# Kernel tuning notes

Hardware: AMD Instinct MI355X
Metric: run time of the kernel (lower is better)

The kernel has to match this reference:

```python
import jax, jax.numpy as jnp
import numpy as np

B, P, E = 256, 196, 2048           # batch, num_pixels, encoder_size
H, A, EMB = 2048, 512, 300         # hidden, attention, embedding dims
V_IN, V_OUT = 262, 261             # input vocab (classes+2), output (classes+1)
T = 7                              # max_seq_len + 2


def setup_inputs() -> dict:
    key = jax.random.key(0)
    ks = jax.random.split(key, 20)
    s = 0.02
    return {
        "encoder_feature_out": jax.random.normal(ks[0], (B, P, E), jnp.float32),
        "encoder_out": jax.random.normal(ks[1], (B, E), jnp.float32),
        "annotations_X": jax.random.randint(ks[2], (B, T), 0, V_IN),
        "is_train": 1,
        "emb_W": jax.random.normal(ks[3], (V_IN, EMB), jnp.float32) * s,
        "feat_W": jax.random.normal(ks[4], (H, E), jnp.float32) * s,
        "feat_b": jnp.zeros((H,), jnp.float32),
        "W_ih": jax.random.normal(ks[5], (4 * H, EMB + E), jnp.float32) * s,
        "W_hh": jax.random.normal(ks[6], (4 * H, H), jnp.float32) * s,
        "b_ih": jnp.zeros((4 * H,), jnp.float32),
        "b_hh": jnp.zeros((4 * H,), jnp.float32),
        "enc_att_W": jax.random.normal(ks[7], (A, E), jnp.float32) * s,
        "enc_att_b": jnp.zeros((A,), jnp.float32),
        "dec_att_W": jax.random.normal(ks[8], (A, H), jnp.float32) * s,
        "dec_att_b": jnp.zeros((A,), jnp.float32),
        "full_att_W": jax.random.normal(ks[9], (1, A), jnp.float32) * s,
        "full_att_b": jnp.zeros((1,), jnp.float32),
        "fbeta_W": jax.random.normal(ks[10], (E, H), jnp.float32) * s,
        "fbeta_b": jnp.zeros((E,), jnp.float32),
        "fc_W": jax.random.normal(ks[11], (V_OUT, H), jnp.float32) * s,
        "fc_b": jnp.zeros((V_OUT,), jnp.float32),
    }


def _forward(encoder_feature_out, encoder_out, annotations_X,
             emb_W, feat_W, feat_b, W_ih, W_hh, b_ih, b_hh,
             enc_att_W, enc_att_b, dec_att_W, dec_att_b,
             full_att_W, full_att_b, fbeta_W, fbeta_b, fc_W, fc_b):
    enc = encoder_feature_out                                  # (B,P,E)
    # encoder side of additive attention is constant across steps
    att1 = jnp.einsum('bpe,ae->bpa', enc, enc_att_W) + enc_att_b  # (B,P,A)
    h0 = encoder_out @ feat_W.T + feat_b                       # (B,H)
    c0 = jnp.zeros_like(h0)

    def step(carry, ann_t):
        h, c = carry
        # additive attention
        att2 = h @ dec_att_W.T + dec_att_b                     # (B,A)
        e = jax.nn.relu(att1 + att2[:, None, :]) @ full_att_W[0] + full_att_b[0]  # (B,P)
        alpha = jax.nn.softmax(e, axis=1)                      # (B,P)
        awe = jnp.einsum('bp,bpe->be', alpha, enc)             # (B,E)
        gate = jax.nn.sigmoid(h @ fbeta_W.T + fbeta_b)         # (B,E)
        awe = gate * awe
        # LSTMCell (dropout layers in eval mode -> identity)
        x = jnp.concatenate([emb_W[ann_t], awe], axis=1)       # (B,EMB+E)
        gates = x @ W_ih.T + b_ih + h @ W_hh.T + b_hh          # (B,4H)
        i, f, g, o = jnp.split(gates, 4, axis=1)
        c = jax.nn.sigmoid(f) * c + jax.nn.sigmoid(i) * jnp.tanh(g)
        h = jax.nn.sigmoid(o) * jnp.tanh(c)
        yhat = h @ fc_W.T + fc_b                               # (B,V_OUT)
        return (h, c), (yhat, alpha)

    _, (yhats, alphas) = jax.lax.scan(step, (h0, c0), annotations_X.T)  # (T,B,...)
    return jnp.transpose(yhats, (1, 0, 2)), jnp.transpose(alphas, (1, 0, 2))


def reference(encoder_feature_out, encoder_out, annotations_X, is_train,
              emb_W, feat_W, feat_b, W_ih, W_hh, b_ih, b_hh,
              enc_att_W, enc_att_b, dec_att_W, dec_att_b,
              full_att_W, full_att_b, fbeta_W, fbeta_b, fc_W, fc_b):
    # is_train=True (teacher forcing) path
    return _forward(encoder_feature_out, encoder_out, annotations_X,
                    emb_W, feat_W, feat_b, W_ih, W_hh, b_ih, b_hh,
                    enc_att_W, enc_att_b, dec_att_W, dec_att_b,
                    full_att_W, full_att_b, fbeta_W, fbeta_b, fc_W, fc_b)
```

## Files before the change

kernel.cpp:

```cpp
#include <hip/hip_runtime.h>
#include <math.h>

#define B_    256
#define P_    196
#define E_    2048
#define H_    2048
#define A_    512
#define EMB_  300
#define VOUT_ 261
#define T_    7

#define KPAD_   4480
#define EMBOFF_ 2048
#define AWEOFF_ 2348
#define KREAL_  4396

#define NSTEP_  2880
#define FCN_    320

typedef __attribute__((ext_vector_type(8))) short          short8_t;
typedef __attribute__((ext_vector_type(8))) unsigned short ushort8_t;
typedef __attribute__((ext_vector_type(4))) float          f32x4;

__device__ __forceinline__ unsigned short f2b(float f) {
    union { float f; unsigned int u; } v; v.f = f;
    unsigned int x = v.u;
    unsigned int r = (x + 0x7fffu + ((x >> 16) & 1u)) >> 16;
    return (unsigned short)r;
}
__device__ __forceinline__ float b2f(unsigned short u) {
    union { unsigned int u; float f; } v; v.u = ((unsigned int)u) << 16;
    return v.f;
}

__global__ __launch_bounds__(256)
void gemm_skinny(const unsigned short* __restrict__ Ab, int lda,
                 const unsigned short* __restrict__ Bw, int ldb,
                 float* __restrict__ Cpart, int N, int Kper)
{
    __shared__ ushort8_t As8[256 * 8];
    __shared__ ushort8_t Bs8[64 * 8];

    const int tid  = threadIdx.x;
    const int lane = tid & 63;
    const int w    = tid >> 6;
    const int col0 = blockIdx.x * 64;
    const int kbase = blockIdx.y * Kper;
    float* __restrict__ Cs = Cpart + (size_t)blockIdx.y * 256 * N;

    const int rb  = tid >> 3;
    const int seg = tid & 7;
    const int swz = seg ^ (rb & 7);

    const unsigned short* Ap = Ab + (size_t)rb * lda + kbase + seg * 8;
    const unsigned short* Bp = Bw + (size_t)(col0 + rb) * ldb + kbase + seg * 8;

    const int lr = lane & 15;
    const int hi = lane >> 4;

    f32x4 acc[4][4];
    #pragma unroll
    for (int m = 0; m < 4; ++m)
        #pragma unroll
        for (int n = 0; n < 4; ++n)
            acc[m][n] = (f32x4){0.f, 0.f, 0.f, 0.f};

    ushort8_t aR[8], bR[2];
    #pragma unroll
    for (int i = 0; i < 8; ++i)
        aR[i] = *(const ushort8_t*)(Ap + (size_t)i * 32 * lda);
    bR[0] = *(const ushort8_t*)(Bp);
    bR[1] = *(const ushort8_t*)(Bp + (size_t)32 * ldb);

    for (int k0 = 0; k0 < Kper; k0 += 64) {
        __syncthreads();
        #pragma unroll
        for (int i = 0; i < 8; ++i)
            As8[(rb + i * 32) * 8 + swz] = aR[i];
        Bs8[rb * 8 + swz]        = bR[0];
        Bs8[(rb + 32) * 8 + swz] = bR[1];
        __syncthreads();
        if (k0 + 64 < Kper) {
            #pragma unroll
            for (int i = 0; i < 8; ++i)
                aR[i] = *(const ushort8_t*)(Ap + (size_t)i * 32 * lda + k0 + 64);
            bR[0] = *(const ushort8_t*)(Bp + k0 + 64);
            bR[1] = *(const ushort8_t*)(Bp + (size_t)32 * ldb + k0 + 64);
        }
        #pragma unroll
        for (int kc = 0; kc < 2; ++kc) {
            short8_t af[4], bf[4];
            #pragma unroll
            for (int m = 0; m < 4; ++m) {
                const int row = w * 64 + m * 16 + lr;
                af[m] = *(const short8_t*)&As8[row * 8 + ((kc * 4 + hi) ^ (row & 7))];
            }
            #pragma unroll
            for (int n = 0; n < 4; ++n) {
                const int row = n * 16 + lr;
                bf[n] = *(const short8_t*)&Bs8[row * 8 + ((kc * 4 + hi) ^ (row & 7))];
            }
            #pragma unroll
            for (int m = 0; m < 4; ++m)
                #pragma unroll
                for (int n = 0; n < 4; ++n)
                    acc[m][n] = __builtin_amdgcn_mfma_f32_16x16x32_bf16(
                        af[m], bf[n], acc[m][n], 0, 0, 0);
        }
    }

    #pragma unroll
    for (int m = 0; m < 4; ++m) {
        const int grow0 = w * 64 + m * 16 + hi * 4;
        #pragma unroll
        for (int n = 0; n < 4; ++n) {
            const int gcol = col0 + n * 16 + lr;
            #pragma unroll
            for (int r = 0; r < 4; ++r)
                Cs[(size_t)(grow0 + r) * N + gcol] = acc[m][n][r];
        }
    }
}

template<bool ABF16>
__global__ __launch_bounds__(256)
void gemm_mfma(const void* __restrict__ Ap, int lda,
               const unsigned short* __restrict__ Bw, int ldb,
               unsigned short* __restrict__ Cp, int ldc,
               const float* __restrict__ bias,
               int M, int N, int K)
{
    __shared__ __align__(16) unsigned short As[64][40];
    __shared__ __align__(16) unsigned short Bs[128][40];

    const int tid  = threadIdx.x;
    const int lane = tid & 63;
    const int wid  = tid >> 6;
    const int wr   = wid >> 1;
    const int wc   = wid & 1;
    const int row0 = blockIdx.y * 64;
    const int col0 = blockIdx.x * 128;

    const int ar = tid >> 2;
    const int as = (tid & 3) * 8;
    const int br = tid >> 1;
    const int bs = (tid & 1) * 16;

    const int lr = lane & 15;
    const int lk = (lane >> 4) * 8;

    f32x4 acc[2][4];
    #pragma unroll
    for (int m = 0; m < 2; ++m)
        #pragma unroll
        for (int n = 0; n < 4; ++n)
            acc[m][n] = (f32x4){0.f, 0.f, 0.f, 0.f};

    for (int k0 = 0; k0 < K; k0 += 32) {
        ushort8_t aval = {0,0,0,0,0,0,0,0};
        if (row0 + ar < M) {
            if (ABF16) {
                const unsigned short* A16 = (const unsigned short*)Ap;
                aval = *(const ushort8_t*)(A16 + (size_t)(row0 + ar) * lda + k0 + as);
            } else {
                const float* Af = (const float*)Ap;
                const float* p = Af + (size_t)(row0 + ar) * lda + k0 + as;
                float4 v0 = *(const float4*)(p);
                float4 v1 = *(const float4*)(p + 4);
                aval[0] = f2b(v0.x); aval[1] = f2b(v0.y);
                aval[2] = f2b(v0.z); aval[3] = f2b(v0.w);
                aval[4] = f2b(v1.x); aval[5] = f2b(v1.y);
                aval[6] = f2b(v1.z); aval[7] = f2b(v1.w);
            }
        }
        ushort8_t bv0 = {0,0,0,0,0,0,0,0}, bv1 = {0,0,0,0,0,0,0,0};
        if (col0 + br < N) {
            const unsigned short* p = Bw + (size_t)(col0 + br) * ldb + k0 + bs;
            bv0 = *(const ushort8_t*)(p);
            bv1 = *(const ushort8_t*)(p + 8);
        }
        __syncthreads();
        *(ushort8_t*)&As[ar][as]     = aval;
        *(ushort8_t*)&Bs[br][bs]     = bv0;
        *(ushort8_t*)&Bs[br][bs + 8] = bv1;
        __syncthreads();

        short8_t af[2], bf[4];
        #pragma unroll
        for (int m = 0; m < 2; ++m)
            af[m] = *(const short8_t*)&As[wr * 32 + m * 16 + lr][lk];
        #pragma unroll
        for (int n = 0; n < 4; ++n)
            bf[n] = *(const short8_t*)&Bs[wc * 64 + n * 16 + lr][lk];
        #pragma unroll
        for (int m = 0; m < 2; ++m)
            #pragma unroll
            for (int n = 0; n < 4; ++n)
                acc[m][n] = __builtin_amdgcn_mfma_f32_16x16x32_bf16(
                    af[m], bf[n], acc[m][n], 0, 0, 0);
    }

    #pragma unroll
    for (int m = 0; m < 2; ++m) {
        const int grow0 = row0 + wr * 32 + m * 16 + (lane >> 4) * 4;
        #pragma unroll
        for (int n = 0; n < 4; ++n) {
            const int gcol = col0 + wc * 64 + n * 16 + lr;
            if (gcol >= N) continue;
            const float bv = bias[gcol];
            #pragma unroll
            for (int r = 0; r < 4; ++r) {
                const int grow = grow0 + r;
                if (grow >= M) continue;
                Cp[(size_t)grow * ldc + gcol] = f2b(acc[m][n][r] + bv);
            }
        }
    }
}

__global__ __launch_bounds__(256)
void cvt_bf16_kernel(const float* __restrict__ in, unsigned short* __restrict__ out,
                     int n8)
{
    const int idx = blockIdx.x * 256 + threadIdx.x;
    if (idx >= n8) return;
    const size_t base = (size_t)idx * 8;
    float4 v0 = *(const float4*)(in + base);
    float4 v1 = *(const float4*)(in + base + 4);
    ushort8_t u;
    u[0]=f2b(v0.x); u[1]=f2b(v0.y); u[2]=f2b(v0.z); u[3]=f2b(v0.w);
    u[4]=f2b(v1.x); u[5]=f2b(v1.y); u[6]=f2b(v1.z); u[7]=f2b(v1.w);
    *(ushort8_t*)(out + base) = u;
}

__global__ __launch_bounds__(256)
void build_wcat_kernel(const float* __restrict__ W_ih, const float* __restrict__ W_hh,
                       unsigned short* __restrict__ wcat)
{
    const int row = blockIdx.x;
    for (int s = threadIdx.x; s < KPAD_ / 8; s += 256) {
        const int k0 = s * 8;
        ushort8_t u;
        if (k0 + 8 <= H_) {
            const float* p = W_hh + (size_t)row * H_ + k0;
            float4 v0 = *(const float4*)(p);
            float4 v1 = *(const float4*)(p + 4);
            u[0]=f2b(v0.x); u[1]=f2b(v0.y); u[2]=f2b(v0.z); u[3]=f2b(v0.w);
            u[4]=f2b(v1.x); u[5]=f2b(v1.y); u[6]=f2b(v1.z); u[7]=f2b(v1.w);
        } else if (k0 >= H_ && k0 + 8 <= KREAL_) {
            const float* p = W_ih + (size_t)row * (EMB_ + E_) + (k0 - H_);
            float4 v0 = *(const float4*)(p);
            float4 v1 = *(const float4*)(p + 4);
            u[0]=f2b(v0.x); u[1]=f2b(v0.y); u[2]=f2b(v0.z); u[3]=f2b(v0.w);
            u[4]=f2b(v1.x); u[5]=f2b(v1.y); u[6]=f2b(v1.z); u[7]=f2b(v1.w);
        } else {
            #pragma unroll
            for (int i = 0; i < 8; ++i) {
                const int k = k0 + i;
                float v = 0.f;
                if (k < KREAL_ && k >= H_) v = W_ih[(size_t)row * (EMB_ + E_) + (k - H_)];
                u[i] = f2b(v);
            }
        }
        *(ushort8_t*)(wcat + (size_t)row * KPAD_ + k0) = u;
    }
}

__global__ __launch_bounds__(256)
void build_wstep_kernel(const float* __restrict__ dec_attW,
                        const float* __restrict__ fbeta_W,
                        const float* __restrict__ fc_W,
                        unsigned short* __restrict__ wstep)
{
    const int row = blockIdx.x;
    const int c0  = threadIdx.x * 8;
    const float* src;
    if (row < A_)                 src = dec_attW + (size_t)row * H_ + c0;
    else if (row < A_ + E_)       src = fbeta_W + (size_t)(row - A_) * H_ + c0;
    else if (row < A_ + E_ + VOUT_) src = fc_W + (size_t)(row - A_ - E_) * H_ + c0;
    else                          src = nullptr;
    ushort8_t u = {0,0,0,0,0,0,0,0};
    if (src) {
        float4 v0 = *(const float4*)(src);
        float4 v1 = *(const float4*)(src + 4);
        u[0]=f2b(v0.x); u[1]=f2b(v0.y); u[2]=f2b(v0.z); u[3]=f2b(v0.w);
        u[4]=f2b(v1.x); u[5]=f2b(v1.y); u[6]=f2b(v1.z); u[7]=f2b(v1.w);
    }
    *(ushort8_t*)(wstep + (size_t)row * H_ + c0) = u;
}

__global__ __launch_bounds__(256)
void reduce_step(const float* __restrict__ parts, float* __restrict__ att2,
                 float* __restrict__ gatelin, float* __restrict__ outy,
                 const float* __restrict__ dec_attb, const float* __restrict__ fbeta_b,
                 const float* __restrict__ fc_b, int t)
{
    const int i = blockIdx.x * 256 + threadIdx.x;
    const int row = i / NSTEP_;
    const int col = i - row * NSTEP_;
    float acc = 0.f;
    #pragma unroll
    for (int s = 0; s < 8; ++s)
        acc += parts[(size_t)s * 256 * NSTEP_ + i];
    if (col < A_) {
        att2[row * A_ + col] = acc + dec_attb[col];
    } else if (col < A_ + E_) {
        const int c = col - A_;
        gatelin[(size_t)row * E_ + c] = acc + fbeta_b[c];
    } else {
        const int c = col - (A_ + E_);
        if (c < VOUT_ && t > 0)
            outy[(size_t)row * T_ * VOUT_ + (size_t)(t - 1) * VOUT_ + c] = acc + fc_b[c];
    }
}

__global__ __launch_bounds__(256)
void reduce_h0(const float* __restrict__ parts, const float* __restrict__ bias,
               unsigned short* __restrict__ xcat)
{
    const int i = blockIdx.x * 256 + threadIdx.x;
    const int row = i >> 11, col = i & (H_ - 1);
    float acc = bias[col];
    #pragma unroll
    for (int s = 0; s < 8; ++s)
        acc += parts[(size_t)s * 256 * H_ + i];
    xcat[(size_t)row * KPAD_ + col] = f2b(acc);
}

__global__ __launch_bounds__(256)
void e_kernel(const unsigned short* __restrict__ att1, const float* __restrict__ att2,
              const float* __restrict__ fw, const float* __restrict__ fb,
              float* __restrict__ e)
{
    const int wid  = threadIdx.x >> 6;
    const int lane = threadIdx.x & 63;
    const int row  = blockIdx.x * 4 + wid;
    const int b    = row / P_;
    const unsigned short* a1 = att1 + (size_t)row * A_;
    const float* a2 = att2 + (size_t)b * A_;
    float acc = 0.f;
    #pragma unroll
    for (int a = lane; a < A_; a += 64) {
        float v = b2f(a1[a]) + a2[a];
        v = v > 0.f ? v : 0.f;
        acc = fmaf(v, fw[a], acc);
    }
    #pragma unroll
    for (int off = 32; off > 0; off >>= 1)
        acc += __shfl_down(acc, off);
    if (lane == 0) e[row] = acc + fb[0];
}

__global__ __launch_bounds__(256)
void softmax_kernel(const float* __restrict__ e, float* __restrict__ alpha,
                    float* __restrict__ out_alpha, int t)
{
    const int b   = blockIdx.x;
    const int tid = threadIdx.x;
    const int wid = tid >> 6, lane = tid & 63;
    __shared__ float red[4];

    float v = (tid < P_) ? e[b * P_ + tid] : -1e30f;

    float m = v;
    #pragma unroll
    for (int off = 32; off > 0; off >>= 1)
        m = fmaxf(m, __shfl_xor(m, off));
    if (lane == 0) red[wid] = m;
    __syncthreads();
    m = fmaxf(fmaxf(red[0], red[1]), fmaxf(red[2], red[3]));
    __syncthreads();

    float p = (tid < P_) ? expf(v - m) : 0.f;
    float s = p;
    #pragma unroll
    for (int off = 32; off > 0; off >>= 1)
        s += __shfl_xor(s, off);
    if (lane == 0) red[wid] = s;
    __syncthreads();
    s = red[0] + red[1] + red[2] + red[3];

    if (tid < P_) {
        const float a = p / s;
        alpha[b * P_ + tid] = a;
        out_alpha[((size_t)b * T_ + t) * P_ + tid] = a;
    }
}

__global__ __launch_bounds__(256)
void awe_kernel(const float* __restrict__ alpha,
                const float* __restrict__ encf, const unsigned short* __restrict__ enc16,
                int use16,
                const float* __restrict__ gatelin, unsigned short* __restrict__ xcat)
{
    const int b  = blockIdx.y;
    const int ei = blockIdx.x * 256 + threadIdx.x;
    __shared__ float al[P_];
    if (threadIdx.x < P_) al[threadIdx.x] = alpha[b * P_ + threadIdx.x];
    __syncthreads();

    float acc = 0.f;
    if (use16) {
        const unsigned short* ep = enc16 + (size_t)b * P_ * E_ + ei;
        #pragma unroll 4
        for (int p = 0; p < P_; ++p)
            acc = fmaf(al[p], b2f(ep[(size_t)p * E_]), acc);
    } else {
        const float* ep = encf + (size_t)b * P_ * E_ + ei;
        #pragma unroll 4
        for (int p = 0; p < P_; ++p)
            acc = fmaf(al[p], ep[(size_t)p * E_], acc);
    }

    const float g  = gatelin[(size_t)b * E_ + ei];
    const float sg = 1.f / (1.f + expf(-g));
    xcat[(size_t)b * KPAD_ + AWEOFF_ + ei] = f2b(sg * acc);
}

__global__ __launch_bounds__(256)
void lstm_kernel(const float* __restrict__ parts, const float* __restrict__ bias4h,
                 float* __restrict__ c, unsigned short* __restrict__ xcat)
{
    const int idx = blockIdx.x * 256 + threadIdx.x;
    const int b = idx >> 11;
    const int j = idx & (H_ - 1);
    const float* p0 = parts + (size_t)b * 4 * H_;
    const float* p1 = p0 + (size_t)256 * 4 * H_;
    const float gi = bias4h[j]          + p0[j]          + p1[j];
    const float gf = bias4h[H_ + j]     + p0[H_ + j]     + p1[H_ + j];
    const float gg = bias4h[2 * H_ + j] + p0[2 * H_ + j] + p1[2 * H_ + j];
    const float go = bias4h[3 * H_ + j] + p0[3 * H_ + j] + p1[3 * H_ + j];
    const float si = 1.f / (1.f + expf(-gi));
    const float sf = 1.f / (1.f + expf(-gf));
    const float so = 1.f / (1.f + expf(-go));
    const float cn = sf * c[idx] + si * tanhf(gg);
    c[idx] = cn;
    xcat[(size_t)b * KPAD_ + j] = f2b(so * tanhf(cn));
}

__global__ __launch_bounds__(256)
void gather_kernel(const int* __restrict__ ann, const float* __restrict__ embW,
                   unsigned short* __restrict__ xcat, int t)
{
    const int b = blockIdx.x;
    const int r = ann[b * T_ + t];
    for (int j = threadIdx.x; j < EMB_; j += 256)
        xcat[(size_t)b * KPAD_ + EMBOFF_ + j] = f2b(embW[(size_t)r * EMB_ + j]);
}

__global__ __launch_bounds__(256)
void addvec_kernel(const float* __restrict__ a, const float* __restrict__ b,
                   float* __restrict__ o, int n)
{
    const int i = blockIdx.x * 256 + threadIdx.x;
    if (i < n) o[i] = a[i] + b[i];
}

extern "C" void kernel_launch(void* const* d_in, const int* in_sizes, int n_in,
                              void* d_out, int out_size, void* d_ws, size_t ws_size,
                              hipStream_t stream)
{
    const float* enc      = (const float*)d_in[0];
    const float* enc_out  = (const float*)d_in[1];
    const int*   ann      = (const int*)  d_in[2];
    const float* emb_W    = (const float*)d_in[4];
    const float* feat_W   = (const float*)d_in[5];
    const float* feat_b   = (const float*)d_in[6];
    const float* W_ih     = (const float*)d_in[7];
    const float* W_hh     = (const float*)d_in[8];
    const float* b_ih     = (const float*)d_in[9];
    const float* b_hh     = (const float*)d_in[10];
    const float* enc_attW = (const float*)d_in[11];
    const float* enc_attb = (const float*)d_in[12];
    const float* dec_attW = (const float*)d_in[13];
    const float* dec_attb = (const float*)d_in[14];
    const float* full_attW= (const float*)d_in[15];
    const float* full_attb= (const float*)d_in[16];
    const float* fbeta_W  = (const float*)d_in[17];
    const float* fbeta_b  = (const float*)d_in[18];
    const float* fc_W     = (const float*)d_in[19];
    const float* fc_b     = (const float*)d_in[20];
    (void)in_sizes; (void)n_in; (void)out_size;

    float* out   = (float*)d_out;
    float* out_y = out;
    float* out_a = out + (size_t)B_ * T_ * VOUT_;

    char* base = (char*)d_ws;
    size_t off = 0;
    auto alloc = [&](size_t bytes) -> char* {
        char* p = base + off;
        off += (bytes + 255) & ~(size_t)255;
        return p;
    };
    unsigned short* att1_16   = (unsigned short*)alloc((size_t)B_ * P_ * A_ * 2);
    unsigned short* wcat16    = (unsigned short*)alloc((size_t)4 * H_ * KPAD_ * 2);
    unsigned short* wstep16   = (unsigned short*)alloc((size_t)NSTEP_ * H_ * 2);
    unsigned short* encattW16 = (unsigned short*)alloc((size_t)A_ * E_ * 2);
    unsigned short* featW16   = (unsigned short*)alloc((size_t)H_ * E_ * 2);
    unsigned short* encout16  = (unsigned short*)alloc((size_t)B_ * E_ * 2);
    unsigned short* xcat16    = (unsigned short*)alloc((size_t)B_ * KPAD_ * 2);
    float* cbuf    = (float*)alloc((size_t)B_ * H_ * 4);
    float* att2buf = (float*)alloc((size_t)B_ * A_ * 4);
    float* ebuf    = (float*)alloc((size_t)B_ * P_ * 4);
    float* alpha   = (float*)alloc((size_t)B_ * P_ * 4);
    float* gatelin = (float*)alloc((size_t)B_ * E_ * 4);
    float* bias4h  = (float*)alloc((size_t)4 * H_ * 4);
    float* parts   = (float*)alloc((size_t)8 * B_ * NSTEP_ * 4);
    const size_t enc_elems = (size_t)B_ * P_ * E_;
    const int use16 = (off + enc_elems * 2 <= ws_size) ? 1 : 0;
    unsigned short* enc16 = use16 ? (unsigned short*)alloc(enc_elems * 2) : nullptr;

    const dim3 blk(256);

    addvec_kernel<<<dim3((4 * H_ + 255) / 256), blk, 0, stream>>>(b_ih, b_hh, bias4h, 4 * H_);
    cvt_bf16_kernel<<<dim3((A_ * E_ / 8 + 255) / 256), blk, 0, stream>>>(enc_attW, encattW16, A_ * E_ / 8);
    cvt_bf16_kernel<<<dim3((H_ * E_ / 8 + 255) / 256), blk, 0, stream>>>(feat_W, featW16, H_ * E_ / 8);
    cvt_bf16_kernel<<<dim3((B_ * E_ / 8 + 255) / 256), blk, 0, stream>>>(enc_out, encout16, B_ * E_ / 8);
    build_wcat_kernel<<<dim3(4 * H_), blk, 0, stream>>>(W_ih, W_hh, wcat16);
    build_wstep_kernel<<<dim3(NSTEP_), blk, 0, stream>>>(dec_attW, fbeta_W, fc_W, wstep16);
    hipMemsetAsync(xcat16, 0, (size_t)B_ * KPAD_ * 2, stream);
    hipMemsetAsync(cbuf, 0, (size_t)B_ * H_ * 4, stream);
    if (use16)
        cvt_bf16_kernel<<<dim3((int)(enc_elems / 8 + 255) / 256), blk, 0, stream>>>(enc, enc16, (int)(enc_elems / 8));

    {
        dim3 g((A_ + 127) / 128, (B_ * P_) / 64);
        if (use16)
            gemm_mfma<true><<<g, blk, 0, stream>>>(enc16, E_, encattW16, E_,
                att1_16, A_, enc_attb, B_ * P_, A_, E_);
        else
            gemm_mfma<false><<<g, blk, 0, stream>>>(enc, E_, encattW16, E_,
                att1_16, A_, enc_attb, B_ * P_, A_, E_);
    }
    gemm_skinny<<<dim3(H_ / 64, 8), blk, 0, stream>>>(encout16, E_, featW16, E_,
                                                      parts, H_, E_ / 8);
    reduce_h0<<<dim3(B_ * H_ / 256), blk, 0, stream>>>(parts, feat_b, xcat16);

    for (int t = 0; t <= T_; ++t) {
        gemm_skinny<<<dim3(NSTEP_ / 64, 8), blk, 0, stream>>>(xcat16, KPAD_, wstep16, H_,
                                                              parts, NSTEP_, H_ / 8);
        reduce_step<<<dim3(B_ * NSTEP_ / 256), blk, 0, stream>>>(parts, att2buf, gatelin,
            out_y, dec_attb, fbeta_b, fc_b, t);
        if (t == T_) break;

        e_kernel<<<dim3(B_ * P_ / 4), blk, 0, stream>>>(att1_16, att2buf, full_attW, full_attb, ebuf);
        softmax_kernel<<<dim3(B_), blk, 0, stream>>>(ebuf, alpha, out_a, t);
        awe_kernel<<<dim3(E_ / 256, B_), blk, 0, stream>>>(alpha, enc, enc16, use16,
                                                           gatelin, xcat16);
        gather_kernel<<<dim3(B_), blk, 0, stream>>>(ann, emb_W, xcat16, t);

        gemm_skinny<<<dim3(4 * H_ / 64, 2), blk, 0, stream>>>(xcat16, KPAD_, wcat16, KPAD_,
                                                              parts, 4 * H_, KPAD_ / 2);
        lstm_kernel<<<dim3(B_ * H_ / 256), blk, 0, stream>>>(parts, bias4h, cbuf, xcat16);
    }
}
```

Measured before the change: 1.362 ms.

## Fuse per-step reduction, attention, softmax, awe and gather; reuse skinny GEMM for att1

```diff
diff --git a/kernel.cpp b/kernel.cpp
--- a/kernel.cpp
+++ b/kernel.cpp
@@ -12,11 +12,10 @@
 
 #define KPAD_   4480
 #define EMBOFF_ 2048
-#define AWEOFF_ 2348
-#define KREAL_  4396
+#define AWEOFF_ 2352
 
 #define NSTEP_  2880
-#define FCN_    320
+#define FCOFF_  2560
 
 typedef __attribute__((ext_vector_type(8))) short          short8_t;
 typedef __attribute__((ext_vector_type(8))) unsigned short ushort8_t;
@@ -33,10 +32,12 @@
     return v.f;
 }
 
-__global__ __launch_bounds__(256)
-void gemm_skinny(const unsigned short* __restrict__ Ab, int lda,
-                 const unsigned short* __restrict__ Bw, int ldb,
-                 float* __restrict__ Cpart, int N, int Kper)
+template<bool SPLITK, bool OUT16>
+__global__ __launch_bounds__(256)
+void gemm_sk(const unsigned short* __restrict__ Ab, int lda,
+             const unsigned short* __restrict__ Bw, int ldb,
+             void* __restrict__ Cout, int ldc,
+             int Kper, int colbase, const float* __restrict__ bias)
 {
     __shared__ ushort8_t As8[256 * 8];
     __shared__ ushort8_t Bs8[64 * 8];
@@ -44,15 +45,15 @@
     const int tid  = threadIdx.x;
     const int lane = tid & 63;
     const int w    = tid >> 6;
-    const int col0 = blockIdx.x * 64;
-    const int kbase = blockIdx.y * Kper;
-    float* __restrict__ Cs = Cpart + (size_t)blockIdx.y * 256 * N;
+    const int col0 = colbase + blockIdx.x * 64;
+    const int kbase = SPLITK ? blockIdx.y * Kper : 0;
+    const int mrow0 = SPLITK ? 0 : blockIdx.y * 256;
 
     const int rb  = tid >> 3;
     const int seg = tid & 7;
     const int swz = seg ^ (rb & 7);
 
-    const unsigned short* Ap = Ab + (size_t)rb * lda + kbase + seg * 8;
+    const unsigned short* Ap = Ab + (size_t)(mrow0 + rb) * lda + kbase + seg * 8;
     const unsigned short* Bp = Bw + (size_t)(col0 + rb) * ldb + kbase + seg * 8;
 
     const int lr = lane & 15;
@@ -109,15 +110,32 @@
         }
     }
 
-    #pragma unroll
-    for (int m = 0; m < 4; ++m) {
-        const int grow0 = w * 64 + m * 16 + hi * 4;
-        #pragma unroll
-        for (int n = 0; n < 4; ++n) {
-            const int gcol = col0 + n * 16 + lr;
-            #pragma unroll
-            for (int r = 0; r < 4; ++r)
-                Cs[(size_t)(grow0 + r) * N + gcol] = acc[m][n][r];
+    if (OUT16) {
+        unsigned short* C16 = (unsigned short*)Cout;
+        #pragma unroll
+        for (int m = 0; m < 4; ++m) {
+            const int grow0 = mrow0 + w * 64 + m * 16 + hi * 4;
+            #pragma unroll
+            for (int n = 0; n < 4; ++n) {
+                const int gcol = col0 + n * 16 + lr;
+                const float bv = bias[gcol];
+                #pragma unroll
+                for (int r = 0; r < 4; ++r)
+                    C16[(size_t)(grow0 + r) * ldc + gcol] = f2b(acc[m][n][r] + bv);
+            }
+        }
+    } else {
+        float* Cs = (float*)Cout + (SPLITK ? (size_t)blockIdx.y * 256 * ldc : 0);
+        #pragma unroll
+        for (int m = 0; m < 4; ++m) {
+            const int grow0 = w * 64 + m * 16 + hi * 4;
+            #pragma unroll
+            for (int n = 0; n < 4; ++n) {
+                const int gcol = col0 + n * 16 + lr;
+                #pragma unroll
+                for (int r = 0; r < 4; ++r)
+                    Cs[(size_t)(grow0 + r) * ldc + gcol] = acc[m][n][r];
+            }
         }
     }
 }
@@ -238,19 +256,17 @@
                        unsigned short* __restrict__ wcat)
 {
     const int row = blockIdx.x;
+    const int LIH = EMB_ + E_;
     for (int s = threadIdx.x; s < KPAD_ / 8; s += 256) {
         const int k0 = s * 8;
         ushort8_t u;
-        if (k0 + 8 <= H_) {
-            const float* p = W_hh + (size_t)row * H_ + k0;
-            float4 v0 = *(const float4*)(p);
-            float4 v1 = *(const float4*)(p + 4);
-            u[0]=f2b(v0.x); u[1]=f2b(v0.y); u[2]=f2b(v0.z); u[3]=f2b(v0.w);
-            u[4]=f2b(v1.x); u[5]=f2b(v1.y); u[6]=f2b(v1.z); u[7]=f2b(v1.w);
-        } else if (k0 >= H_ && k0 + 8 <= KREAL_) {
-            const float* p = W_ih + (size_t)row * (EMB_ + E_) + (k0 - H_);
-            float4 v0 = *(const float4*)(p);
-            float4 v1 = *(const float4*)(p + 4);
+        const float* src = nullptr;
+        if (k0 + 8 <= H_)                        src = W_hh + (size_t)row * H_ + k0;
+        else if (k0 >= H_ && k0 + 8 <= 2344)     src = W_ih + (size_t)row * LIH + (k0 - H_);
+        else if (k0 >= AWEOFF_ && k0 + 8 <= 4400) src = W_ih + (size_t)row * LIH + (k0 - 2052);
+        if (src) {
+            float4 v0 = *(const float4*)(src);
+            float4 v1 = *(const float4*)(src + 4);
             u[0]=f2b(v0.x); u[1]=f2b(v0.y); u[2]=f2b(v0.z); u[3]=f2b(v0.w);
             u[4]=f2b(v1.x); u[5]=f2b(v1.y); u[6]=f2b(v1.z); u[7]=f2b(v1.w);
         } else {
@@ -258,7 +274,8 @@
             for (int i = 0; i < 8; ++i) {
                 const int k = k0 + i;
                 float v = 0.f;
-                if (k < KREAL_ && k >= H_) v = W_ih[(size_t)row * (EMB_ + E_) + (k - H_)];
+                if (k >= H_ && k < 2348)              v = W_ih[(size_t)row * LIH + (k - H_)];
+                else if (k >= AWEOFF_ && k < 4400)    v = W_ih[(size_t)row * LIH + (k - 2052)];
                 u[i] = f2b(v);
             }
         }
@@ -275,10 +292,10 @@
     const int row = blockIdx.x;
     const int c0  = threadIdx.x * 8;
     const float* src;
-    if (row < A_)                 src = dec_attW + (size_t)row * H_ + c0;
-    else if (row < A_ + E_)       src = fbeta_W + (size_t)(row - A_) * H_ + c0;
+    if (row < A_)                   src = dec_attW + (size_t)row * H_ + c0;
+    else if (row < A_ + E_)         src = fbeta_W + (size_t)(row - A_) * H_ + c0;
     else if (row < A_ + E_ + VOUT_) src = fc_W + (size_t)(row - A_ - E_) * H_ + c0;
-    else                          src = nullptr;
+    else                            src = nullptr;
     ushort8_t u = {0,0,0,0,0,0,0,0};
     if (src) {
         float4 v0 = *(const float4*)(src);
@@ -290,31 +307,6 @@
 }
 
 __global__ __launch_bounds__(256)
-void reduce_step(const float* __restrict__ parts, float* __restrict__ att2,
-                 float* __restrict__ gatelin, float* __restrict__ outy,
-                 const float* __restrict__ dec_attb, const float* __restrict__ fbeta_b,
-                 const float* __restrict__ fc_b, int t)
-{
-    const int i = blockIdx.x * 256 + threadIdx.x;
-    const int row = i / NSTEP_;
-    const int col = i - row * NSTEP_;
-    float acc = 0.f;
-    #pragma unroll
-    for (int s = 0; s < 8; ++s)
-        acc += parts[(size_t)s * 256 * NSTEP_ + i];
-    if (col < A_) {
-        att2[row * A_ + col] = acc + dec_attb[col];
-    } else if (col < A_ + E_) {
-        const int c = col - A_;
-        gatelin[(size_t)row * E_ + c] = acc + fbeta_b[c];
-    } else {
-        const int c = col - (A_ + E_);
-        if (c < VOUT_ && t > 0)
-            outy[(size_t)row * T_ * VOUT_ + (size_t)(t - 1) * VOUT_ + c] = acc + fc_b[c];
-    }
-}
-
-__global__ __launch_bounds__(256)
 void reduce_h0(const float* __restrict__ parts, const float* __restrict__ bias,
                unsigned short* __restrict__ xcat)
 {
@@ -328,40 +320,55 @@
 }
 
 __global__ __launch_bounds__(256)
-void e_kernel(const unsigned short* __restrict__ att1, const float* __restrict__ att2,
-              const float* __restrict__ fw, const float* __restrict__ fb,
-              float* __restrict__ e)
-{
-    const int wid  = threadIdx.x >> 6;
-    const int lane = threadIdx.x & 63;
-    const int row  = blockIdx.x * 4 + wid;
-    const int b    = row / P_;
-    const unsigned short* a1 = att1 + (size_t)row * A_;
-    const float* a2 = att2 + (size_t)b * A_;
-    float acc = 0.f;
-    #pragma unroll
-    for (int a = lane; a < A_; a += 64) {
-        float v = b2f(a1[a]) + a2[a];
-        v = v > 0.f ? v : 0.f;
-        acc = fmaf(v, fw[a], acc);
-    }
-    #pragma unroll
-    for (int off = 32; off > 0; off >>= 1)
-        acc += __shfl_down(acc, off);
-    if (lane == 0) e[row] = acc + fb[0];
-}
-
-__global__ __launch_bounds__(256)
-void softmax_kernel(const float* __restrict__ e, float* __restrict__ alpha,
-                    float* __restrict__ out_alpha, int t)
-{
-    const int b   = blockIdx.x;
+void fused_att(const float* __restrict__ parts, const float* __restrict__ dec_attb,
+               const unsigned short* __restrict__ att1,
+               const float* __restrict__ fw_g, const float* __restrict__ fb,
+               float* __restrict__ alpha, float* __restrict__ out_a, int t)
+{
+    const int b = blockIdx.x;
     const int tid = threadIdx.x;
-    const int wid = tid >> 6, lane = tid & 63;
+    const int lane = tid & 63;
+    const int wid  = tid >> 6;
+    __shared__ float att2s[A_];
+    __shared__ float es[P_];
     __shared__ float red[4];
 
-    float v = (tid < P_) ? e[b * P_ + tid] : -1e30f;
-
+    #pragma unroll
+    for (int it = 0; it < A_ / 256; ++it) {
+        const int c = tid + it * 256;
+        float acc = dec_attb[c];
+        #pragma unroll
+        for (int s = 0; s < 8; ++s)
+            acc += parts[((size_t)s * B_ + b) * NSTEP_ + c];
+        att2s[c] = acc;
+    }
+    __syncthreads();
+
+    float a2r[8], fwr[8];
+    #pragma unroll
+    for (int k = 0; k < 8; ++k) {
+        a2r[k] = att2s[lane * 8 + k];
+        fwr[k] = fw_g[lane * 8 + k];
+    }
+    const float fbv = fb[0];
+
+    for (int p = wid; p < P_; p += 4) {
+        ushort8_t v = *(const ushort8_t*)(att1 + ((size_t)b * P_ + p) * A_ + lane * 8);
+        float acc = 0.f;
+        #pragma unroll
+        for (int k = 0; k < 8; ++k) {
+            float x = b2f(v[k]) + a2r[k];
+            x = x > 0.f ? x : 0.f;
+            acc = fmaf(x, fwr[k], acc);
+        }
+        #pragma unroll
+        for (int off = 32; off > 0; off >>= 1)
+            acc += __shfl_xor(acc, off);
+        if (lane == 0) es[p] = acc + fbv;
+    }
+    __syncthreads();
+
+    float v = (tid < P_) ? es[tid] : -1e30f;
     float m = v;
     #pragma unroll
     for (int off = 32; off > 0; off >>= 1)
@@ -370,7 +377,6 @@
     __syncthreads();
     m = fmaxf(fmaxf(red[0], red[1]), fmaxf(red[2], red[3]));
     __syncthreads();
-
     float p = (tid < P_) ? expf(v - m) : 0.f;
     float s = p;
     #pragma unroll
@@ -379,42 +385,84 @@
     if (lane == 0) red[wid] = s;
     __syncthreads();
     s = red[0] + red[1] + red[2] + red[3];
-
     if (tid < P_) {
         const float a = p / s;
         alpha[b * P_ + tid] = a;
-        out_alpha[((size_t)b * T_ + t) * P_ + tid] = a;
-    }
-}
-
-__global__ __launch_bounds__(256)
-void awe_kernel(const float* __restrict__ alpha,
-                const float* __restrict__ encf, const unsigned short* __restrict__ enc16,
-                int use16,
-                const float* __restrict__ gatelin, unsigned short* __restrict__ xcat)
-{
-    const int b  = blockIdx.y;
-    const int ei = blockIdx.x * 256 + threadIdx.x;
+        out_a[((size_t)b * T_ + t) * P_ + tid] = a;
+    }
+}
+
+__global__ __launch_bounds__(256)
+void fused_awe(const float* __restrict__ parts, const float* __restrict__ fbeta_b,
+               const float* __restrict__ alpha,
+               const float* __restrict__ encf, const unsigned short* __restrict__ enc16,
+               int use16,
+               const int* __restrict__ ann, const float* __restrict__ embW,
+               unsigned short* __restrict__ xcat, int t)
+{
+    const int b = blockIdx.x;
+    const int tid = threadIdx.x;
     __shared__ float al[P_];
-    if (threadIdx.x < P_) al[threadIdx.x] = alpha[b * P_ + threadIdx.x];
+    if (tid < P_) al[tid] = alpha[b * P_ + tid];
     __syncthreads();
 
-    float acc = 0.f;
+    const int e0 = tid * 8;
+    float g[8];
+    #pragma unroll
+    for (int k = 0; k < 8; ++k) {
+        float acc = fbeta_b[e0 + k];
+        #pragma unroll
+        for (int s = 0; s < 8; ++s)
+            acc += parts[((size_t)s * B_ + b) * NSTEP_ + A_ + e0 + k];
+        g[k] = 1.f / (1.f + expf(-acc));
+    }
+
+    float acc[8] = {0.f,0.f,0.f,0.f,0.f,0.f,0.f,0.f};
     if (use16) {
-        const unsigned short* ep = enc16 + (size_t)b * P_ * E_ + ei;
-        #pragma unroll 4
-        for (int p = 0; p < P_; ++p)
-            acc = fmaf(al[p], b2f(ep[(size_t)p * E_]), acc);
+        const unsigned short* ep = enc16 + (size_t)b * P_ * E_ + e0;
+        for (int p = 0; p < P_; p += 2) {
+            ushort8_t v0 = *(const ushort8_t*)(ep + (size_t)p * E_);
+            ushort8_t v1 = *(const ushort8_t*)(ep + (size_t)(p + 1) * E_);
+            const float a0 = al[p], a1 = al[p + 1];
+            #pragma unroll
+            for (int k = 0; k < 8; ++k)
+                acc[k] = fmaf(a1, b2f(v1[k]), fmaf(a0, b2f(v0[k]), acc[k]));
+        }
     } else {
-        const float* ep = encf + (size_t)b * P_ * E_ + ei;
-        #pragma unroll 4
-        for (int p = 0; p < P_; ++p)
-            acc = fmaf(al[p], ep[(size_t)p * E_], acc);
-    }
-
-    const float g  = gatelin[(size_t)b * E_ + ei];
-    const float sg = 1.f / (1.f + expf(-g));
-    xcat[(size_t)b * KPAD_ + AWEOFF_ + ei] = f2b(sg * acc);
+        const float* ep = encf + (size_t)b * P_ * E_ + e0;
+        for (int p = 0; p < P_; ++p) {
+            float4 v0 = *(const float4*)(ep + (size_t)p * E_);
+            float4 v1 = *(const float4*)(ep + (size_t)p * E_ + 4);
+            const float a0 = al[p];
+            acc[0] = fmaf(a0, v0.x, acc[0]); acc[1] = fmaf(a0, v0.y, acc[1]);
+            acc[2] = fmaf(a0, v0.z, acc[2]); acc[3] = fmaf(a0, v0.w, acc[3]);
+            acc[4] = fmaf(a0, v1.x, acc[4]); acc[5] = fmaf(a0, v1.y, acc[5]);
+            acc[6] = fmaf(a0, v1.z, acc[6]); acc[7] = fmaf(a0, v1.w, acc[7]);
+        }
+    }
+    ushort8_t o;
+    #pragma unroll
+    for (int k = 0; k < 8; ++k) o[k] = f2b(g[k] * acc[k]);
+    *(ushort8_t*)(xcat + (size_t)b * KPAD_ + AWEOFF_ + e0) = o;
+
+    const int r = ann[b * T_ + t];
+    for (int j = tid; j < EMB_; j += 256)
+        xcat[(size_t)b * KPAD_ + EMBOFF_ + j] = f2b(embW[(size_t)r * EMB_ + j]);
+}
+
+__global__ __launch_bounds__(256)
+void fc_reduce(const float* __restrict__ parts, const float* __restrict__ fc_b,
+               float* __restrict__ out_y, int tm1)
+{
+    const int i = blockIdx.x * 256 + threadIdx.x;
+    if (i >= B_ * VOUT_) return;
+    const int b = i / VOUT_;
+    const int c = i - b * VOUT_;
+    float acc = fc_b[c];
+    #pragma unroll
+    for (int s = 0; s < 8; ++s)
+        acc += parts[((size_t)s * B_ + b) * NSTEP_ + FCOFF_ + c];
+    out_y[((size_t)b * T_ + tm1) * VOUT_ + c] = acc;
 }
 
 __global__ __launch_bounds__(256)
@@ -436,16 +484,6 @@
     const float cn = sf * c[idx] + si * tanhf(gg);
     c[idx] = cn;
     xcat[(size_t)b * KPAD_ + j] = f2b(so * tanhf(cn));
-}
-
-__global__ __launch_bounds__(256)
-void gather_kernel(const int* __restrict__ ann, const float* __restrict__ embW,
-                   unsigned short* __restrict__ xcat, int t)
-{
-    const int b = blockIdx.x;
-    const int r = ann[b * T_ + t];
-    for (int j = threadIdx.x; j < EMB_; j += 256)
-        xcat[(size_t)b * KPAD_ + EMBOFF_ + j] = f2b(embW[(size_t)r * EMB_ + j]);
 }
 
 __global__ __launch_bounds__(256)
@@ -501,10 +539,7 @@
     unsigned short* encout16  = (unsigned short*)alloc((size_t)B_ * E_ * 2);
     unsigned short* xcat16    = (unsigned short*)alloc((size_t)B_ * KPAD_ * 2);
     float* cbuf    = (float*)alloc((size_t)B_ * H_ * 4);
-    float* att2buf = (float*)alloc((size_t)B_ * A_ * 4);
-    float* ebuf    = (float*)alloc((size_t)B_ * P_ * 4);
     float* alpha   = (float*)alloc((size_t)B_ * P_ * 4);
-    float* gatelin = (float*)alloc((size_t)B_ * E_ * 4);
     float* bias4h  = (float*)alloc((size_t)4 * H_ * 4);
     float* parts   = (float*)alloc((size_t)8 * B_ * NSTEP_ * 4);
     const size_t enc_elems = (size_t)B_ * P_ * E_;
@@ -524,34 +559,37 @@
     if (use16)
         cvt_bf16_kernel<<<dim3((int)(enc_elems / 8 + 255) / 256), blk, 0, stream>>>(enc, enc16, (int)(enc_elems / 8));
 
-    {
+    if (use16) {
+        dim3 g(A_ / 64, (B_ * P_) / 256);
+        gemm_sk<false, true><<<g, blk, 0, stream>>>(enc16, E_, encattW16, E_,
+            att1_16, A_, E_, 0, enc_attb);
+    } else {
         dim3 g((A_ + 127) / 128, (B_ * P_) / 64);
-        if (use16)
-            gemm_mfma<true><<<g, blk, 0, stream>>>(enc16, E_, encattW16, E_,
-                att1_16, A_, enc_attb, B_ * P_, A_, E_);
+        gemm_mfma<false><<<g, blk, 0, stream>>>(enc, E_, encattW16, E_,
+            att1_16, A_, enc_attb, B_ * P_, A_, E_);
+    }
+    gemm_sk<true, false><<<dim3(H_ / 64, 8), blk, 0, stream>>>(encout16, E_, featW16, E_,
+        parts, H_, E_ / 8, 0, nullptr);
+    reduce_h0<<<dim3(B_ * H_ / 256), blk, 0, stream>>>(parts, feat_b, xcat16);
+
+    for (int t = 0; t <= T_; ++t) {
+        if (t < T_)
+            gemm_sk<true, false><<<dim3(NSTEP_ / 64, 8), blk, 0, stream>>>(
+                xcat16, KPAD_, wstep16, H_, parts, NSTEP_, H_ / 8, 0, nullptr);
         else
-            gemm_mfma<false><<<g, blk, 0, stream>>>(enc, E_, encattW16, E_,
-                att1_16, A_, enc_attb, B_ * P_, A_, E_);
-    }
-    gemm_skinny<<<dim3(H_ / 64, 8), blk, 0, stream>>>(encout16, E_, featW16, E_,
-                                                      parts, H_, E_ / 8);
-    reduce_h0<<<dim3(B_ * H_ / 256), blk, 0, stream>>>(parts, feat_b, xcat16);
-
-    for (int t = 0; t <= T_; ++t) {
-        gemm_skinny<<<dim3(NSTEP_ / 64, 8), blk, 0, stream>>>(xcat16, KPAD_, wstep16, H_,
-                                                              parts, NSTEP_, H_ / 8);
-        reduce_step<<<dim3(B_ * NSTEP_ / 256), blk, 0, stream>>>(parts, att2buf, gatelin,
-            out_y, dec_attb, fbeta_b, fc_b, t);
+            gemm_sk<true, false><<<dim3((NSTEP_ - FCOFF_) / 64, 8), blk, 0, stream>>>(
+                xcat16, KPAD_, wstep16, H_, parts, NSTEP_, H_ / 8, FCOFF_, nullptr);
+        if (t > 0)
+            fc_reduce<<<dim3((B_ * VOUT_ + 255) / 256), blk, 0, stream>>>(parts, fc_b, out_y, t - 1);
         if (t == T_) break;
 
-        e_kernel<<<dim3(B_ * P_ / 4), blk, 0, stream>>>(att1_16, att2buf, full_attW, full_attb, ebuf);
-        softmax_kernel<<<dim3(B_), blk, 0, stream>>>(ebuf, alpha, out_a, t);
-        awe_kernel<<<dim3(E_ / 256, B_), blk, 0, stream>>>(alpha, enc, enc16, use16,
-                                                           gatelin, xcat16);
-        gather_kernel<<<dim3(B_), blk, 0, stream>>>(ann, emb_W, xcat16, t);
-
-        gemm_skinny<<<dim3(4 * H_ / 64, 2), blk, 0, stream>>>(xcat16, KPAD_, wcat16, KPAD_,
-                                                              parts, 4 * H_, KPAD_ / 2);
+        fused_att<<<dim3(B_), blk, 0, stream>>>(parts, dec_attb, att1_16,
+                                                full_attW, full_attb, alpha, out_a, t);
+        fused_awe<<<dim3(B_), blk, 0, stream>>>(parts, fbeta_b, alpha, enc, enc16,
+                                                use16, ann, emb_W, xcat16, t);
+
+        gemm_sk<true, false><<<dim3(4 * H_ / 64, 2), blk, 0, stream>>>(
+            xcat16, KPAD_, wcat16, KPAD_, parts, 4 * H_, KPAD_ / 2, 0, nullptr);
         lstm_kernel<<<dim3(B_ * H_ / 256), blk, 0, stream>>>(parts, bias4h, cbuf, xcat16);
     }
 }
```

Result: slower. 1.458 ms (+7.0%).
